# Optimization experiments

Hardware: AMD Instinct MI355X
Metric: run time of the kernel (lower is better)

## Reference

```python
import jax, jax.numpy as jnp
import numpy as np

D_MODEL, N_HEADS, N_KV_HEADS = 2048, 16, 4
D_HEAD = D_MODEL // N_HEADS  # 128
N_REP = N_HEADS // N_KV_HEADS  # 4
B, S = 2, 2048
ROPE_THETA = 10000.0


def setup_inputs() -> dict:
    key = jax.random.key(0)
    ks = jax.random.split(key, 6)
    x = jax.random.normal(ks[0], (B, S, D_MODEL), dtype=jnp.float32)
    # RoPE frequencies (real/imag parts of freqs_cis)
    inv_freq = 1.0 / (ROPE_THETA ** (np.arange(0, D_HEAD, 2, dtype=np.float32) / D_HEAD))
    angles = np.arange(S, dtype=np.float32)[:, None] * inv_freq[None, :]  # [S, D_HEAD//2]
    freqs_cos = jnp.asarray(np.cos(angles))
    freqs_sin = jnp.asarray(np.sin(angles))
    # causal additive mask [1,1,S,S]
    causal = jnp.tril(jnp.ones((S, S), dtype=bool))
    mask = jnp.where(causal, 0.0, -1e9).astype(jnp.float32)[None, None]
    scale = 0.02
    wq = jax.random.normal(ks[1], (D_MODEL, N_HEADS * D_HEAD), dtype=jnp.float32) * scale
    wk = jax.random.normal(ks[2], (D_MODEL, N_KV_HEADS * D_HEAD), dtype=jnp.float32) * scale
    wv = jax.random.normal(ks[3], (D_MODEL, N_KV_HEADS * D_HEAD), dtype=jnp.float32) * scale
    wo = jax.random.normal(ks[4], (N_HEADS * D_HEAD, D_MODEL), dtype=jnp.float32) * scale
    return {"x": x, "freqs_cos": freqs_cos, "freqs_sin": freqs_sin, "mask": mask,
            "wq": wq, "wk": wk, "wv": wv, "wo": wo}


def _apply_rope(t, cos, sin):
    # t: [B, S, H, D]; cos/sin: [S, D//2] -> complex rotation on interleaved pairs
    tr = t.reshape(*t.shape[:-1], -1, 2)
    xr, xi = tr[..., 0], tr[..., 1]
    c = cos[None, :, None, :]
    s = sin[None, :, None, :]
    out_r = xr * c - xi * s
    out_i = xr * s + xi * c
    return jnp.stack([out_r, out_i], axis=-1).reshape(t.shape)


def reference(x, freqs_cos, freqs_sin, mask, wq, wk, wv, wo):
    b, s, _ = x.shape
    xq = (x @ wq).reshape(b, s, N_HEADS, D_HEAD)
    xk = (x @ wk).reshape(b, s, N_KV_HEADS, D_HEAD)
    xv = (x @ wv).reshape(b, s, N_KV_HEADS, D_HEAD)
    xq = _apply_rope(xq, freqs_cos, freqs_sin)
    xk = _apply_rope(xk, freqs_cos, freqs_sin)
    # GQA: repeat each kv head n_rep times (head h uses kv head h // n_rep)
    xk = jnp.repeat(xk, N_REP, axis=2)  # [B,S,H,D]
    xv = jnp.repeat(xv, N_REP, axis=2)
    scores = jnp.einsum("bshd,bthd->bhst", xq, xk) / jnp.sqrt(jnp.float32(D_HEAD))
    scores = scores + mask
    probs = jax.nn.softmax(scores, axis=-1)
    out = jnp.einsum("bhst,bthd->bshd", probs, xv).reshape(b, s, N_HEADS * D_HEAD)
    return out @ wo
```

## Files before the change

kernel.cpp:

```cpp
#include <hip/hip_runtime.h>
#include <hip/hip_bf16.h>

#define BB 2
#define SS 2048
#define DM 2048
#define NH 16
#define NKV 4
#define DH 128
#define QS 3072

typedef __hip_bfloat16 bf16;
typedef short short4v __attribute__((ext_vector_type(4)));
typedef short short8 __attribute__((ext_vector_type(8)));
typedef float floatx4 __attribute__((ext_vector_type(4)));

#if __has_builtin(__builtin_amdgcn_exp2f)
#define EX2(x) __builtin_amdgcn_exp2f(x)
#else
#define EX2(x) exp2f(x)
#endif

__device__ __forceinline__ bf16 f2b(float v) { return __float2bfloat16(v); }
__device__ __forceinline__ short f2bs(float v) {
    bf16 t = __float2bfloat16(v);
    return __builtin_bit_cast(short, t);
}
__device__ __forceinline__ void store_c(bf16* p, float v) { *p = __float2bfloat16(v); }
__device__ __forceinline__ void store_c(float* p, float v) { *p = v; }

__global__ __launch_bounds__(256) void convert_x(const float4* __restrict__ x,
                                                 bf16* __restrict__ xb, int n4) {
    int i = blockIdx.x * blockDim.x + threadIdx.x;
    if (i >= n4) return;
    float4 v = x[i];
    short4v o;
    o.x = f2bs(v.x); o.y = f2bs(v.y); o.z = f2bs(v.z); o.w = f2bs(v.w);
    *(short4v*)(xb + (size_t)i * 4) = o;
}

__global__ __launch_bounds__(256) void convert_wT(const float* __restrict__ w,
                                                  bf16* __restrict__ outT,
                                                  int N, int Kd) {
    const int n0 = blockIdx.x * 64, k0 = blockIdx.y * 64;
    __shared__ float tile[64][65];
    const int tid = threadIdx.x;
    for (int i = tid; i < 4096; i += 256) {
        int r = i >> 6, c = i & 63;
        tile[r][c] = w[(size_t)(k0 + r) * N + n0 + c];
    }
    __syncthreads();
    for (int i = tid; i < 4096; i += 256) {
        int r = i >> 6, c = i & 63;
        outT[(size_t)(n0 + r) * Kd + k0 + c] = f2b(tile[c][r]);
    }
}

__global__ __launch_bounds__(256) void convert_wqkv(const float* __restrict__ wq,
                                                    const float* __restrict__ wk,
                                                    const float* __restrict__ wv,
                                                    bf16* __restrict__ outT) {
    const int bx = blockIdx.x;
    const float* w; int N; int n0;
    if (bx < 32)      { w = wq; N = 2048; n0 = bx * 64; }
    else if (bx < 40) { w = wk; N = 512;  n0 = (bx - 32) * 64; }
    else              { w = wv; N = 512;  n0 = (bx - 40) * 64; }
    const int k0 = blockIdx.y * 64;
    const int gn0 = bx * 64;
    __shared__ float tile[64][65];
    const int tid = threadIdx.x;
    for (int i = tid; i < 4096; i += 256) {
        int r = i >> 6, c = i & 63;
        tile[r][c] = w[(size_t)(k0 + r) * N + n0 + c];
    }
    __syncthreads();
    for (int i = tid; i < 4096; i += 256) {
        int r = i >> 6, c = i & 63;
        outT[(size_t)(gn0 + r) * DM + k0 + c] = f2b(tile[c][r]);
    }
}

template <typename TC>
__global__ __launch_bounds__(256) void mfma_gemm(const bf16* __restrict__ A,
                                                 const bf16* __restrict__ BT,
                                                 TC* __restrict__ C,
                                                 int M, int N, int K) {
    __shared__ short As[3][128 * 32];
    __shared__ short Bs[3][128 * 32];
    const int tid = threadIdx.x;
    const int w = tid >> 6, lane = tid & 63;
    const int col16 = lane & 15, quad = lane >> 4;
    const int gx = gridDim.x;
    const int nwg = gx * gridDim.y;
    int lin = blockIdx.y * gx + blockIdx.x;
    lin = (lin & 7) * (nwg >> 3) + (lin >> 3);
    const int row0 = (lin / gx) * 128, col0 = (lin % gx) * 128;
    const int wr0 = (w >> 1) * 64, wc0 = (w & 1) * 64;
    const int nt = K / 32;

    auto issue = [&](int t, int b) {
        const int k0 = t * 32;
        #pragma unroll
        for (int it = 0; it < 2; it++) {
            int cc = w * 128 + it * 64 + lane;
            int r = cc >> 2, seg = cc & 3;
            const bf16* g = A + (size_t)(row0 + r) * K + k0 + ((seg ^ (r & 3)) * 8);
            __builtin_amdgcn_global_load_lds(
                (const __attribute__((address_space(1))) unsigned int*)g,
                (__attribute__((address_space(3))) unsigned int*)&As[b][(w * 128 + it * 64) * 8],
                16, 0, 0);
        }
        #pragma unroll
        for (int it = 0; it < 2; it++) {
            int cc = w * 128 + it * 64 + lane;
            int r = cc >> 2, seg = cc & 3;
            const bf16* g = BT + (size_t)(col0 + r) * K + k0 + ((seg ^ (r & 3)) * 8);
            __builtin_amdgcn_global_load_lds(
                (const __attribute__((address_space(1))) unsigned int*)g,
                (__attribute__((address_space(3))) unsigned int*)&Bs[b][(w * 128 + it * 64) * 8],
                16, 0, 0);
        }
    };

    floatx4 acc[4][4];
    #pragma unroll
    for (int mi = 0; mi < 4; mi++)
        #pragma unroll
        for (int ni = 0; ni < 4; ni++) acc[mi][ni] = (floatx4){0.f, 0.f, 0.f, 0.f};

    issue(0, 0);
    if (1 < nt) issue(1, 1);

    for (int t = 0; t < nt; ++t) {
        const int cb = t % 3;
        if (t + 1 < nt) { asm volatile("s_waitcnt vmcnt(4)" ::: "memory"); }
        else            { asm volatile("s_waitcnt vmcnt(0)" ::: "memory"); }
        __builtin_amdgcn_s_barrier();
        if (t + 2 < nt) issue(t + 2, (t + 2) % 3);

        short8 af[4], bfr[4];
        #pragma unroll
        for (int mi = 0; mi < 4; mi++) {
            int r = wr0 + mi * 16 + col16;
            af[mi] = *(const short8*)&As[cb][r * 32 + ((quad ^ (r & 3)) * 8)];
        }
        #pragma unroll
        for (int ni = 0; ni < 4; ni++) {
            int r = wc0 + ni * 16 + col16;
            bfr[ni] = *(const short8*)&Bs[cb][r * 32 + ((quad ^ (r & 3)) * 8)];
        }
        #pragma unroll
        for (int mi = 0; mi < 4; mi++)
            #pragma unroll
            for (int ni = 0; ni < 4; ni++)
                acc[mi][ni] = __builtin_amdgcn_mfma_f32_16x16x32_bf16(af[mi], bfr[ni], acc[mi][ni], 0, 0, 0);
    }
    #pragma unroll
    for (int mi = 0; mi < 4; mi++)
        #pragma unroll
        for (int ni = 0; ni < 4; ni++)
            #pragma unroll
            for (int r = 0; r < 4; r++)
                store_c(&C[(size_t)(row0 + wr0 + mi * 16 + quad * 4 + r) * N +
                           col0 + wc0 + ni * 16 + col16],
                        acc[mi][ni][r]);
}

__global__ void rope_all(bf16* __restrict__ qkv, const float* __restrict__ cs,
                         const float* __restrict__ sn, int totq, int total) {
    int idx = blockIdx.x * blockDim.x + threadIdx.x;
    if (idx >= total) return;
    bf16* base; int n_heads; int rel;
    if (idx < totq) { base = qkv;        n_heads = NH;  rel = idx; }
    else            { base = qkv + 2048; n_heads = NKV; rel = idx - totq; }
    int i = rel & 63;
    int h = (rel >> 6) % n_heads;
    size_t bs = (size_t)rel / (64 * n_heads);
    int s = (int)(bs % SS);
    float c = cs[s * 64 + i];
    float si = sn[s * 64 + i];
    bf16* p = base + bs * QS + h * DH + 2 * i;
    float xr = __bfloat162float(p[0]), xi = __bfloat162float(p[1]);
    p[0] = f2b(xr * c - xi * si);
    p[1] = f2b(xr * si + xi * c);
}

__global__ __launch_bounds__(256) void transpose_v(const bf16* __restrict__ qkv,
                                                   bf16* __restrict__ vt) {
    const int s0 = blockIdx.x * 64, d0 = blockIdx.y * 64;
    const int b = blockIdx.z >> 2, kvh = blockIdx.z & 3;
    __shared__ bf16 tile[64][65];
    const int tid = threadIdx.x;
    for (int i = tid; i < 4096; i += 256) {
        int r = i >> 6, c = i & 63;
        tile[r][c] = qkv[(size_t)(b * SS + s0 + r) * QS + 2560 + kvh * DH + d0 + c];
    }
    __syncthreads();
    for (int i = tid; i < 4096; i += 256) {
        int r = i >> 6, c = i & 63;
        vt[((size_t)(b * NKV + kvh) * DH + d0 + r) * SS + s0 + c] = tile[c][r];
    }
}

#define PPAD 88

__global__ __launch_bounds__(256) void flash_attn(const bf16* __restrict__ qkv,
                                                  const bf16* __restrict__ vt,
                                                  bf16* __restrict__ ao) {
    const int bx = blockIdx.x, h = blockIdx.y, b = blockIdx.z;
    const int kvh = h >> 2;
    __shared__ short Ks[2][64 * 128];
    __shared__ short Vs[2][128 * 64];
    __shared__ short Ps[4 * 16 * PPAD];
    const int tid = threadIdx.x;
    const int w = tid >> 6, lane = tid & 63;
    const int col = lane & 15, quad = lane >> 4;
    const int c7 = col & 7;
    const float C = 0.12751746517859245f;
    const float THR_RAW = 90.5f;

    const int krl = lane >> 4, kseg = lane & 15;
    const int vrl = lane >> 3, vseg = lane & 7;

    const bf16* kgb = qkv + (size_t)b * SS * QS + 2048 + kvh * DH;
    const bf16* vgb = vt + (size_t)(b * NKV + kvh) * DH * SS;

    const short8 vone = {0x3F80, 0x3F80, 0x3F80, 0x3F80, 0x3F80, 0x3F80, 0x3F80, 0x3F80};

    for (int phase = 0; phase < 2; phase++) {
        const int qt = phase == 0 ? bx : (SS / 64 - 1 - bx);
        const int q0 = qt * 64;

        short8 aq[4];
        const bf16* qbase = qkv + (size_t)(b * SS + q0 + w * 16 + col) * QS + h * DH;
        #pragma unroll
        for (int kc = 0; kc < 4; kc++)
            aq[kc] = *(const short8*)(qbase + kc * 32 + quad * 8);

        floatx4 o[8];
        #pragma unroll
        for (int dt = 0; dt < 8; dt++) o[dt] = (floatx4){0.f, 0.f, 0.f, 0.f};
        floatx4 oL = (floatx4){0.f, 0.f, 0.f, 0.f};
        float mrow[4] = {-3e38f, -3e38f, -3e38f, -3e38f};

        for (int kt = 0; kt <= qt; kt++) {
            const int cur = kt & 1;
            __syncthreads();
            if (kt == 0) {
                #pragma unroll
                for (int it = 0; it < 4; it++) {
                    int row = w * 16 + it * 4 + krl;
                    const bf16* g = kgb + (size_t)row * QS + ((kseg ^ (row & 7)) * 8);
                    __builtin_amdgcn_global_load_lds(
                        (const __attribute__((address_space(1))) unsigned int*)g,
                        (__attribute__((address_space(3))) unsigned int*)&Ks[0][(w * 16 + it * 4) * 128],
                        16, 0, 0);
                }
                #pragma unroll
                for (int it = 0; it < 4; it++) {
                    int drow = w * 32 + it * 8 + vrl;
                    const bf16* g = vgb + (size_t)drow * SS + ((vseg ^ (drow & 7)) * 8);
                    __builtin_amdgcn_global_load_lds(
                        (const __attribute__((address_space(1))) unsigned int*)g,
                        (__attribute__((address_space(3))) unsigned int*)&Vs[0][(w * 32 + it * 8) * 64],
                        16, 0, 0);
                }
                __syncthreads();
            }
            if (kt < qt) {
                const int nk0 = (kt + 1) * 64;
                #pragma unroll
                for (int it = 0; it < 4; it++) {
                    int row = w * 16 + it * 4 + krl;
                    const bf16* g = kgb + (size_t)(nk0 + row) * QS + ((kseg ^ (row & 7)) * 8);
                    __builtin_amdgcn_global_load_lds(
                        (const __attribute__((address_space(1))) unsigned int*)g,
                        (__attribute__((address_space(3))) unsigned int*)&Ks[cur ^ 1][(w * 16 + it * 4) * 128],
                        16, 0, 0);
                }
                #pragma unroll
                for (int it = 0; it < 4; it++) {
                    int drow = w * 32 + it * 8 + vrl;
                    const bf16* g = vgb + (size_t)drow * SS + nk0 + ((vseg ^ (drow & 7)) * 8);
                    __builtin_amdgcn_global_load_lds(
                        (const __attribute__((address_space(1))) unsigned int*)g,
                        (__attribute__((address_space(3))) unsigned int*)&Vs[cur ^ 1][(w * 32 + it * 8) * 64],
                        16, 0, 0);
                }
            }

            const int k0 = kt * 64;
            floatx4 s[4];
            __builtin_amdgcn_s_setprio(1);
            #pragma unroll
            for (int n = 0; n < 4; n++) {
                s[n] = (floatx4){0.f, 0.f, 0.f, 0.f};
                #pragma unroll
                for (int kc = 0; kc < 4; kc++) {
                    short8 bk = *(const short8*)&Ks[cur][(n * 16 + col) * 128 + (((kc * 4 + quad) ^ c7) * 8)];
                    s[n] = __builtin_amdgcn_mfma_f32_16x16x32_bf16(aq[kc], bk, s[n], 0, 0, 0);
                }
            }
            __builtin_amdgcn_s_setprio(0);

            if (kt == qt) {
                #pragma unroll
                for (int n = 0; n < 4; n++)
                    #pragma unroll
                    for (int r = 0; r < 4; r++)
                        if ((k0 + n * 16 + col) > (q0 + w * 16 + quad * 4 + r)) s[n][r] = -3e38f;
            }

            float rmx[4];
            #pragma unroll
            for (int r = 0; r < 4; r++) {
                float rm = fmaxf(fmaxf(s[0][r], s[1][r]), fmaxf(s[2][r], s[3][r]));
                rm = fmaxf(rm, __shfl_xor(rm, 1));
                rm = fmaxf(rm, __shfl_xor(rm, 2));
                rm = fmaxf(rm, __shfl_xor(rm, 4));
                rm = fmaxf(rm, __shfl_xor(rm, 8));
                rmx[r] = fmaxf(rm, mrow[r]);
            }
            bool need = (rmx[0] - mrow[0] > THR_RAW) | (rmx[1] - mrow[1] > THR_RAW) |
                        (rmx[2] - mrow[2] > THR_RAW) | (rmx[3] - mrow[3] > THR_RAW);
            if (__any((int)need)) {
                float al[4];
                #pragma unroll
                for (int r = 0; r < 4; r++) {
                    al[r] = EX2((mrow[r] - rmx[r]) * C);
                    mrow[r] = rmx[r];
                }
                #pragma unroll
                for (int dt = 0; dt < 8; dt++)
                    #pragma unroll
                    for (int r = 0; r < 4; r++) o[dt][r] *= al[r];
                #pragma unroll
                for (int r = 0; r < 4; r++) oL[r] *= al[r];
            }
            float mC[4];
            #pragma unroll
            for (int r = 0; r < 4; r++) mC[r] = mrow[r] * C;

            short* pw = &Ps[w * 16 * PPAD];
            #pragma unroll
            for (int n = 0; n < 4; n++)
                #pragma unroll
                for (int r = 0; r < 4; r++)
                    pw[(quad * 4 + r) * PPAD + n * 16 + col] =
                        f2bs(EX2(__builtin_fmaf(s[n][r], C, -mC[r])));

            short8 ap0 = *(const short8*)&pw[col * PPAD + quad * 8];
            short8 ap1 = *(const short8*)&pw[col * PPAD + 32 + quad * 8];
            __builtin_amdgcn_s_setprio(1);
            #pragma unroll
            for (int dt = 0; dt < 8; dt++) {
                short8 bv0 = *(const short8*)&Vs[cur][(dt * 16 + col) * 64 + ((quad ^ c7) * 8)];
                o[dt] = __builtin_amdgcn_mfma_f32_16x16x32_bf16(ap0, bv0, o[dt], 0, 0, 0);
                short8 bv1 = *(const short8*)&Vs[cur][(dt * 16 + col) * 64 + (((quad + 4) ^ c7) * 8)];
                o[dt] = __builtin_amdgcn_mfma_f32_16x16x32_bf16(ap1, bv1, o[dt], 0, 0, 0);
            }
            oL = __builtin_amdgcn_mfma_f32_16x16x32_bf16(ap0, vone, oL, 0, 0, 0);
            oL = __builtin_amdgcn_mfma_f32_16x16x32_bf16(ap1, vone, oL, 0, 0, 0);
            __builtin_amdgcn_s_setprio(0);
        }
        #pragma unroll
        for (int r = 0; r < 4; r++) {
            float inv = 1.f / oL[r];
            int srow = q0 + w * 16 + quad * 4 + r;
            bf16* op = ao + ((size_t)(b * SS + srow) * NH + h) * DH;
            #pragma unroll
            for (int dt = 0; dt < 8; dt++)
                op[dt * 16 + col] = f2b(o[dt][r] * inv);
        }
    }
}

extern "C" void kernel_launch(void* const* d_in, const int* in_sizes, int n_in,
                              void* d_out, int out_size, void* d_ws, size_t ws_size,
                              hipStream_t stream) {
    const float* x  = (const float*)d_in[0];
    const float* fc = (const float*)d_in[1];
    const float* fs = (const float*)d_in[2];
    const float* wq = (const float*)d_in[4];
    const float* wk = (const float*)d_in[5];
    const float* wv = (const float*)d_in[6];
    const float* wo = (const float*)d_in[7];
    float* out = (float*)d_out;

    const int M = BB * SS;
    bf16* qkv    = (bf16*)d_ws;
    bf16* xb     = qkv + (size_t)M * QS;
    bf16* wqkvT  = xb + (size_t)M * DM;
    bf16* ao     = xb;
    bf16* vt     = wqkvT;
    bf16* woT    = qkv;

    dim3 blk(256);
    convert_x<<<(M * DM / 4 + 255) / 256, blk, 0, stream>>>((const float4*)x, xb, M * DM / 4);
    convert_wqkv<<<dim3(QS / 64, DM / 64), blk, 0, stream>>>(wq, wk, wv, wqkvT);

    mfma_gemm<bf16><<<dim3(QS / 128, M / 128), blk, 0, stream>>>(xb, wqkvT, qkv, M, QS, DM);

    const int totq = BB * SS * NH * 64;
    const int totk = BB * SS * NKV * 64;
    rope_all<<<(totq + totk + 255) / 256, blk, 0, stream>>>(qkv, fc, fs, totq, totq + totk);

    transpose_v<<<dim3(SS / 64, DH / 64, BB * NKV), blk, 0, stream>>>(qkv, vt);

    flash_attn<<<dim3(SS / 128, NH, BB), blk, 0, stream>>>(qkv, vt, ao);

    convert_wT<<<dim3(DM / 64, DM / 64), blk, 0, stream>>>(wo, woT, DM, DM);
    mfma_gemm<float><<<dim3(DM / 128, M / 128), blk, 0, stream>>>(ao, woT, out, M, DM, DM);
}
```

Baseline: 338.6 us.

## Process two 64-row query groups per warp to reuse K/V tiles

```diff
diff --git a/kernel.cpp b/kernel.cpp
--- a/kernel.cpp
+++ b/kernel.cpp
@@ -203,9 +203,9 @@
 
 #define PPAD 88
 
-__global__ __launch_bounds__(256) void flash_attn(const bf16* __restrict__ qkv,
-                                                  const bf16* __restrict__ vt,
-                                                  bf16* __restrict__ ao) {
+__global__ __launch_bounds__(256, 2) void flash_attn(const bf16* __restrict__ qkv,
+                                                     const bf16* __restrict__ vt,
+                                                     bf16* __restrict__ ao) {
     const int bx = blockIdx.x, h = blockIdx.y, b = blockIdx.z;
     const int kvh = h >> 2;
     __shared__ short Ks[2][64 * 128];
@@ -227,22 +227,32 @@
     const short8 vone = {0x3F80, 0x3F80, 0x3F80, 0x3F80, 0x3F80, 0x3F80, 0x3F80, 0x3F80};
 
     for (int phase = 0; phase < 2; phase++) {
-        const int qt = phase == 0 ? bx : (SS / 64 - 1 - bx);
-        const int q0 = qt * 64;
-
-        short8 aq[4];
-        const bf16* qbase = qkv + (size_t)(b * SS + q0 + w * 16 + col) * QS + h * DH;
-        #pragma unroll
-        for (int kc = 0; kc < 4; kc++)
-            aq[kc] = *(const short8*)(qbase + kc * 32 + quad * 8);
-
-        floatx4 o[8];
-        #pragma unroll
-        for (int dt = 0; dt < 8; dt++) o[dt] = (floatx4){0.f, 0.f, 0.f, 0.f};
-        floatx4 oL = (floatx4){0.f, 0.f, 0.f, 0.f};
-        float mrow[4] = {-3e38f, -3e38f, -3e38f, -3e38f};
-
-        for (int kt = 0; kt <= qt; kt++) {
+        const int qt = phase == 0 ? bx : (SS / 128 - 1 - bx);
+        const int q0 = qt * 128;
+        const int ntile = 2 * qt + 2;
+
+        short8 aq[2][4];
+        #pragma unroll
+        for (int g = 0; g < 2; g++) {
+            const bf16* qbase = qkv + (size_t)(b * SS + q0 + g * 64 + w * 16 + col) * QS + h * DH;
+            #pragma unroll
+            for (int kc = 0; kc < 4; kc++)
+                aq[g][kc] = *(const short8*)(qbase + kc * 32 + quad * 8);
+        }
+
+        floatx4 o[2][8];
+        floatx4 oL[2];
+        float mrow[2][4];
+        #pragma unroll
+        for (int g = 0; g < 2; g++) {
+            #pragma unroll
+            for (int dt = 0; dt < 8; dt++) o[g][dt] = (floatx4){0.f, 0.f, 0.f, 0.f};
+            oL[g] = (floatx4){0.f, 0.f, 0.f, 0.f};
+            #pragma unroll
+            for (int r = 0; r < 4; r++) mrow[g][r] = -3e38f;
+        }
+
+        for (int kt = 0; kt < ntile; kt++) {
             const int cur = kt & 1;
             __syncthreads();
             if (kt == 0) {
@@ -266,7 +276,7 @@
                 }
                 __syncthreads();
             }
-            if (kt < qt) {
+            if (kt + 1 < ntile) {
                 const int nk0 = (kt + 1) * 64;
                 #pragma unroll
                 for (int it = 0; it < 4; it++) {
@@ -289,88 +299,108 @@
             }
 
             const int k0 = kt * 64;
-            floatx4 s[4];
+            floatx4 s[2][4];
             __builtin_amdgcn_s_setprio(1);
             #pragma unroll
             for (int n = 0; n < 4; n++) {
-                s[n] = (floatx4){0.f, 0.f, 0.f, 0.f};
+                s[0][n] = (floatx4){0.f, 0.f, 0.f, 0.f};
+                s[1][n] = (floatx4){0.f, 0.f, 0.f, 0.f};
                 #pragma unroll
                 for (int kc = 0; kc < 4; kc++) {
                     short8 bk = *(const short8*)&Ks[cur][(n * 16 + col) * 128 + (((kc * 4 + quad) ^ c7) * 8)];
-                    s[n] = __builtin_amdgcn_mfma_f32_16x16x32_bf16(aq[kc], bk, s[n], 0, 0, 0);
+                    s[0][n] = __builtin_amdgcn_mfma_f32_16x16x32_bf16(aq[0][kc], bk, s[0][n], 0, 0, 0);
+                    s[1][n] = __builtin_amdgcn_mfma_f32_16x16x32_bf16(aq[1][kc], bk, s[1][n], 0, 0, 0);
                 }
             }
             __builtin_amdgcn_s_setprio(0);
 
-            if (kt == qt) {
+            if (kt >= 2 * qt) {
                 #pragma unroll
                 for (int n = 0; n < 4; n++)
                     #pragma unroll
                     for (int r = 0; r < 4; r++)
-                        if ((k0 + n * 16 + col) > (q0 + w * 16 + quad * 4 + r)) s[n][r] = -3e38f;
-            }
-
-            float rmx[4];
-            #pragma unroll
-            for (int r = 0; r < 4; r++) {
-                float rm = fmaxf(fmaxf(s[0][r], s[1][r]), fmaxf(s[2][r], s[3][r]));
-                rm = fmaxf(rm, __shfl_xor(rm, 1));
-                rm = fmaxf(rm, __shfl_xor(rm, 2));
-                rm = fmaxf(rm, __shfl_xor(rm, 4));
-                rm = fmaxf(rm, __shfl_xor(rm, 8));
-                rmx[r] = fmaxf(rm, mrow[r]);
-            }
-            bool need = (rmx[0] - mrow[0] > THR_RAW) | (rmx[1] - mrow[1] > THR_RAW) |
-                        (rmx[2] - mrow[2] > THR_RAW) | (rmx[3] - mrow[3] > THR_RAW);
-            if (__any((int)need)) {
-                float al[4];
+                        if ((k0 + n * 16 + col) > (q0 + w * 16 + quad * 4 + r)) s[0][n][r] = -3e38f;
+            }
+            if (kt == 2 * qt + 1) {
+                #pragma unroll
+                for (int n = 0; n < 4; n++)
+                    #pragma unroll
+                    for (int r = 0; r < 4; r++)
+                        if ((k0 + n * 16 + col) > (q0 + 64 + w * 16 + quad * 4 + r)) s[1][n][r] = -3e38f;
+            }
+
+            short8 ap[2][2];
+            short* pw = &Ps[w * 16 * PPAD];
+            #pragma unroll
+            for (int g = 0; g < 2; g++) {
+                float rmx[4];
                 #pragma unroll
                 for (int r = 0; r < 4; r++) {
-                    al[r] = EX2((mrow[r] - rmx[r]) * C);
-                    mrow[r] = rmx[r];
-                }
-                #pragma unroll
-                for (int dt = 0; dt < 8; dt++)
-                    #pragma unroll
-                    for (int r = 0; r < 4; r++) o[dt][r] *= al[r];
-                #pragma unroll
-                for (int r = 0; r < 4; r++) oL[r] *= al[r];
-            }
-            float mC[4];
-            #pragma unroll
-            for (int r = 0; r < 4; r++) mC[r] = mrow[r] * C;
-
-            short* pw = &Ps[w * 16 * PPAD];
-            #pragma unroll
-            for (int n = 0; n < 4; n++)
-                #pragma unroll
-                for (int r = 0; r < 4; r++)
-                    pw[(quad * 4 + r) * PPAD + n * 16 + col] =
-                        f2bs(EX2(__builtin_fmaf(s[n][r], C, -mC[r])));
-
-            short8 ap0 = *(const short8*)&pw[col * PPAD + quad * 8];
-            short8 ap1 = *(const short8*)&pw[col * PPAD + 32 + quad * 8];
+                    float rm = fmaxf(fmaxf(s[g][0][r], s[g][1][r]), fmaxf(s[g][2][r], s[g][3][r]));
+                    rm = fmaxf(rm, __shfl_xor(rm, 1));
+                    rm = fmaxf(rm, __shfl_xor(rm, 2));
+                    rm = fmaxf(rm, __shfl_xor(rm, 4));
+                    rm = fmaxf(rm, __shfl_xor(rm, 8));
+                    rmx[r] = fmaxf(rm, mrow[g][r]);
+                }
+                bool need = (rmx[0] - mrow[g][0] > THR_RAW) | (rmx[1] - mrow[g][1] > THR_RAW) |
+                            (rmx[2] - mrow[g][2] > THR_RAW) | (rmx[3] - mrow[g][3] > THR_RAW);
+                if (__any((int)need)) {
+                    float al[4];
+                    #pragma unroll
+                    for (int r = 0; r < 4; r++) {
+                        al[r] = EX2((mrow[g][r] - rmx[r]) * C);
+                        mrow[g][r] = rmx[r];
+                    }
+                    #pragma unroll
+                    for (int dt = 0; dt < 8; dt++)
+                        #pragma unroll
+                        for (int r = 0; r < 4; r++) o[g][dt][r] *= al[r];
+                    #pragma unroll
+                    for (int r = 0; r < 4; r++) oL[g][r] *= al[r];
+                }
+                float mC[4];
+                #pragma unroll
+                for (int r = 0; r < 4; r++) mC[r] = mrow[g][r] * C;
+
+                #pragma unroll
+                for (int n = 0; n < 4; n++)
+                    #pragma unroll
+                    for (int r = 0; r < 4; r++)
+                        pw[(quad * 4 + r) * PPAD + n * 16 + col] =
+                            f2bs(EX2(__builtin_fmaf(s[g][n][r], C, -mC[r])));
+
+                ap[g][0] = *(const short8*)&pw[col * PPAD + quad * 8];
+                ap[g][1] = *(const short8*)&pw[col * PPAD + 32 + quad * 8];
+            }
+
             __builtin_amdgcn_s_setprio(1);
             #pragma unroll
             for (int dt = 0; dt < 8; dt++) {
                 short8 bv0 = *(const short8*)&Vs[cur][(dt * 16 + col) * 64 + ((quad ^ c7) * 8)];
-                o[dt] = __builtin_amdgcn_mfma_f32_16x16x32_bf16(ap0, bv0, o[dt], 0, 0, 0);
+                o[0][dt] = __builtin_amdgcn_mfma_f32_16x16x32_bf16(ap[0][0], bv0, o[0][dt], 0, 0, 0);
+                o[1][dt] = __builtin_amdgcn_mfma_f32_16x16x32_bf16(ap[1][0], bv0, o[1][dt], 0, 0, 0);
                 short8 bv1 = *(const short8*)&Vs[cur][(dt * 16 + col) * 64 + (((quad + 4) ^ c7) * 8)];
-                o[dt] = __builtin_amdgcn_mfma_f32_16x16x32_bf16(ap1, bv1, o[dt], 0, 0, 0);
-            }
-            oL = __builtin_amdgcn_mfma_f32_16x16x32_bf16(ap0, vone, oL, 0, 0, 0);
-            oL = __builtin_amdgcn_mfma_f32_16x16x32_bf16(ap1, vone, oL, 0, 0, 0);
+                o[0][dt] = __builtin_amdgcn_mfma_f32_16x16x32_bf16(ap[0][1], bv1, o[0][dt], 0, 0, 0);
+                o[1][dt] = __builtin_amdgcn_mfma_f32_16x16x32_bf16(ap[1][1], bv1, o[1][dt], 0, 0, 0);
+            }
+            oL[0] = __builtin_amdgcn_mfma_f32_16x16x32_bf16(ap[0][0], vone, oL[0], 0, 0, 0);
+            oL[0] = __builtin_amdgcn_mfma_f32_16x16x32_bf16(ap[0][1], vone, oL[0], 0, 0, 0);
+            oL[1] = __builtin_amdgcn_mfma_f32_16x16x32_bf16(ap[1][0], vone, oL[1], 0, 0, 0);
+            oL[1] = __builtin_amdgcn_mfma_f32_16x16x32_bf16(ap[1][1], vone, oL[1], 0, 0, 0);
             __builtin_amdgcn_s_setprio(0);
         }
         #pragma unroll
-        for (int r = 0; r < 4; r++) {
-            float inv = 1.f / oL[r];
-            int srow = q0 + w * 16 + quad * 4 + r;
-            bf16* op = ao + ((size_t)(b * SS + srow) * NH + h) * DH;
-            #pragma unroll
-            for (int dt = 0; dt < 8; dt++)
-                op[dt * 16 + col] = f2b(o[dt][r] * inv);
-        }
+        for (int g = 0; g < 2; g++)
+            #pragma unroll
+            for (int r = 0; r < 4; r++) {
+                float inv = 1.f / oL[g][r];
+                int srow = q0 + g * 64 + w * 16 + quad * 4 + r;
+                bf16* op = ao + ((size_t)(b * SS + srow) * NH + h) * DH;
+                #pragma unroll
+                for (int dt = 0; dt < 8; dt++)
+                    op[dt * 16 + col] = f2b(o[g][dt][r] * inv);
+            }
     }
 }
 
@@ -406,7 +436,7 @@
 
     transpose_v<<<dim3(SS / 64, DH / 64, BB * NKV), blk, 0, stream>>>(qkv, vt);
 
-    flash_attn<<<dim3(SS / 128, NH, BB), blk, 0, stream>>>(qkv, vt, ao);
+    flash_attn<<<dim3(SS / 256, NH, BB), blk, 0, stream>>>(qkv, vt, ao);
 
     convert_wT<<<dim3(DM / 64, DM / 64), blk, 0, stream>>>(wo, woT, DM, DM);
     mfma_gemm<float><<<dim3(DM / 128, M / 128), blk, 0, stream>>>(ao, woT, out, M, DM, DM);
```

After: 366.6 us. 1.08x slower.
